# Performance work log

Measured on AMD Instinct MI355X. Metric: run time of the kernel, lower is better.

Reference implementation:

```python
import jax, jax.numpy as jnp
import numpy as np

CHUNK = 128  # time_chunk_size from init_kwargs
EPS = 1e-8


def _forward(v, k, alpha, q):
    # v: (T,B,d), k/alpha/q: (T,B,n)
    T, B, d = v.shape
    n = k.shape[-1]
    nc = T // CHUNK  # T assumed divisible by CHUNK
    vr = v.reshape(nc, CHUNK, B, d)
    kr = k.reshape(nc, CHUNK, B, n)
    ar = alpha.reshape(nc, CHUNK, B, n)
    qr = q.reshape(nc, CHUNK, B, n)

    def step(S_prev, xs):
        vc, kc, ac, qc = xs  # (C,B,d), (C,B,n), ...
        outer = jnp.einsum('tbd,tbn->tbdn', vc, kc)          # (C,B,d,n)
        log_a = jnp.log(jnp.clip(ac, EPS))
        log_cp = jnp.cumsum(log_a, axis=0)                   # (C,B,n)
        cp = jnp.exp(log_cp)
        decay = cp / (cp[-1:] + EPS)                         # normalized per chunk
        S_local = jnp.cumsum(outer * decay[:, :, None, :], axis=0)
        prefix = jnp.exp(log_cp[0])                          # (B,n) decay of first step
        S_local = S_local + (S_prev * prefix[:, None, :])[None]
        y = jnp.einsum('tbdn,tbn->tbd', S_local, qc)         # (C,B,d)
        return S_local[-1], y

    S0 = jnp.zeros((B, d, n), v.dtype)
    _, ys = jax.lax.scan(step, S0, (vr, kr, ar, qr))
    return ys.reshape(T, B, d)


def setup_inputs() -> dict:
    key = jax.random.key(0)
    k1, k2, k3, k4 = jax.random.split(key, 4)
    T, B, d, n = 2048, 4, 256, 256
    return {
        'v': jax.random.normal(k1, (T, B, d), jnp.float32),
        'k': jax.random.normal(k2, (T, B, n), jnp.float32),
        'alpha': jax.random.uniform(k3, (T, B, n), jnp.float32),
        'q': jax.random.normal(k4, (T, B, n), jnp.float32),
    }


def reference(v, k, alpha, q):
    return _forward(v, k, alpha, q)
```

## Files before the change

### kernel.cpp

```cpp
#include <hip/hip_runtime.h>
#include <math.h>

typedef unsigned short u16;
typedef unsigned int u32;
typedef __bf16 bf16x8 __attribute__((ext_vector_type(8)));
typedef float f32x4 __attribute__((ext_vector_type(4)));

#define BB   4
#define DD   256
#define NN   256
#define CH   128
#define NCH  16
#define EPSF 1e-8f

#define WS_QB  0u
#define WS_VT  (4u<<20)
#define WS_WT  (8u<<20)
#define WS_WN  (12u<<20)
#define WS_AST (16u<<20)
#define WS_SPT (18u<<20)
#define WS_PF  (26u<<20)
#define WS_UT  (28u<<20)

__device__ __forceinline__ u16 f2bf(float x) {
  u32 u = __float_as_uint(x);
  u32 r = (u + 0x7fffu + ((u >> 16) & 1u)) >> 16;
  return (u16)r;
}
__device__ __forceinline__ float bf2f(u32 lo16) {
  return __uint_as_float(lo16 << 16);
}

__device__ __forceinline__ void gload16(void* lds, const void* g) {
  __builtin_amdgcn_global_load_lds((const __attribute__((address_space(1))) void*)g,
                                   (__attribute__((address_space(3))) void*)lds, 16, 0, 0);
}

__device__ __forceinline__ void stage_tile(u16* lds, const u16* g, int rowstride) {
  int tid = threadIdx.x;
#pragma unroll
  for (int h = 0; h < 2; h++) {
    int ci = tid + h * 256;
    int r = ci >> 3, sl = ci & 7;
    const u16* src = g + (size_t)r * rowstride + ((sl ^ (r & 7)) << 3);
    gload16(lds + (size_t)ci * 8, src);
  }
}

__device__ __forceinline__ void read_frags(const u16* buf, int rbase, int lane,
                                           bf16x8 (&f)[2][2]) {
#pragma unroll
  for (int i = 0; i < 2; i++)
#pragma unroll
    for (int ks = 0; ks < 2; ks++) {
      int r = rbase + i * 16 + (lane & 15);
      int slot = ((ks << 2) + (lane >> 4)) ^ (r & 7);
      f[i][ks] = *reinterpret_cast<const bf16x8*>(buf + r * 64 + slot * 8);
    }
}

__device__ __forceinline__ void mma_step(const u16* Ab, const u16* Bb, int rm, int cn,
                                         int lane, f32x4 (&acc)[2][2]) {
  bf16x8 a[2][2], b[2][2];
  read_frags(Ab, rm, lane, a);
  read_frags(Bb, cn, lane, b);
#pragma unroll
  for (int mf = 0; mf < 2; mf++)
#pragma unroll
    for (int nf = 0; nf < 2; nf++)
#pragma unroll
      for (int ks = 0; ks < 2; ks++)
        acc[mf][nf] = __builtin_amdgcn_mfma_f32_16x16x32_bf16(a[mf][ks], b[nf][ks],
                                                              acc[mf][nf], 0, 0, 0);
}

__global__ __launch_bounds__(256) void k_prep(const float* __restrict__ q,
                                              const float* __restrict__ v,
                                              const float* __restrict__ kin,
                                              const float* __restrict__ alpha,
                                              u16* __restrict__ qb,
                                              u16* __restrict__ vT,
                                              u16* __restrict__ wT,
                                              u16* __restrict__ wn,
                                              float* __restrict__ pf) {
  __shared__ __align__(16) char smem[64 * 136 * 2];
  int bid = blockIdx.x;
  int tid = threadIdx.x;
  if (bid < 1024) {
    int ng = bid & 15, b = (bid >> 4) & 3, c = bid >> 6;
    int nn = tid & 15, seg = tid >> 4;
    int n = ng * 16 + nn;
    int cb = c * BB + b;
    const int stride = BB * NN;
    size_t gbase = ((size_t)(c * CH + seg * 8) * stride) + b * NN + n;
    float lg[8], kv[8];
    float a0 = 0.f, run = 0.f;
#pragma unroll
    for (int i = 0; i < 8; i++) {
      float av = fmaxf(alpha[gbase + (size_t)i * stride], EPSF);
      kv[i] = kin[gbase + (size_t)i * stride];
      if (i == 0) a0 = av;
      run += __logf(av);
      lg[i] = run;
    }
    float (*tot)[17] = (float(*)[17])smem;
    tot[seg][nn] = run;
    __syncthreads();
    float prefix = 0.f, total = 0.f;
#pragma unroll
    for (int j = 0; j < 16; j++) {
      float tv = tot[j][nn];
      if (j < seg) prefix += tv;
      total += tv;
    }
    float rden = 1.f / (__expf(total) + EPSF);
    union { u16 u[8]; uint4 v4; } pk;
    u16* wnrow = wn + (size_t)cb * (CH * NN) + n;
#pragma unroll
    for (int i = 0; i < 8; i++) {
      float cp = __expf(prefix + lg[i]);
      u16 h = f2bf(kv[i] * (cp * rden));
      pk.u[i] = h;
      wnrow[(size_t)(seg * 8 + i) * NN] = h;
    }
    *(uint4*)(wT + (size_t)cb * (NN * CH) + (size_t)n * CH + seg * 8) = pk.v4;
    if (seg == 0) pf[cb * NN + n] = a0;
  } else if (bid < 1280) {
    int b2 = bid - 1024;
    int dt = b2 & 3, cb = b2 >> 2;
    int c = cb >> 2, b = cb & 3;
    int d0 = dt * 64;
    u16* vt = (u16*)smem;
    int sr = tid >> 4, chd = tid & 15;
#pragma unroll
    for (int p = 0; p < 8; p++) {
      int s = p * 16 + sr;
      float4 x = *(const float4*)&v[((size_t)(c * CH + s) * BB + b) * DD + d0 + chd * 4];
      int dbase = chd * 4;
      vt[(dbase + 0) * 136 + s] = f2bf(x.x);
      vt[(dbase + 1) * 136 + s] = f2bf(x.y);
      vt[(dbase + 2) * 136 + s] = f2bf(x.z);
      vt[(dbase + 3) * 136 + s] = f2bf(x.w);
    }
    __syncthreads();
    int dr = tid >> 2, ch = tid & 3;
    const uint4* srcl = (const uint4*)&vt[dr * 136 + ch * 32];
    uint4 a0 = srcl[0], a1 = srcl[1], a2 = srcl[2], a3 = srcl[3];
    uint4* dst = (uint4*)&vT[((size_t)cb * DD + d0 + dr) * CH + ch * 32];
    dst[0] = a0; dst[1] = a1; dst[2] = a2; dst[3] = a3;
  } else {
    size_t gid = (size_t)(bid - 1280) * 256 + tid;
    const float4* src = (const float4*)q + gid * 2;
    float4 x = src[0], z = src[1];
    union { u16 u[8]; uint4 v4; } pk;
    pk.u[0] = f2bf(x.x); pk.u[1] = f2bf(x.y); pk.u[2] = f2bf(x.z); pk.u[3] = f2bf(x.w);
    pk.u[4] = f2bf(z.x); pk.u[5] = f2bf(z.y); pk.u[6] = f2bf(z.z); pk.u[7] = f2bf(z.w);
    ((uint4*)qb)[gid] = pk.v4;
  }
}

__global__ __launch_bounds__(256) void k_utas(const u16* __restrict__ vT,
                                              const u16* __restrict__ wT,
                                              const u16* __restrict__ qb,
                                              const u16* __restrict__ wn,
                                              u16* __restrict__ utb,
                                              u16* __restrict__ asT) {
  __shared__ u16 Al[2][4096], Bl[2][4096];
  int bid = blockIdx.x;
  int tid = threadIdx.x, lane = tid & 63, wv = tid >> 6;
  int rm = (wv >> 1) * 32, cn = (wv & 1) * 32;
  if (bid < 1024) {
    int nt = bid & 3, dt = (bid >> 2) & 3, cb = bid >> 4;
    const u16* A = vT + ((size_t)cb * DD + dt * 64) * CH;
    const u16* B = wT + ((size_t)cb * NN + nt * 64) * CH;
    f32x4 acc[2][2] = {};
    stage_tile(Al[0], A, CH); stage_tile(Al[1], A + 64, CH);
    stage_tile(Bl[0], B, CH); stage_tile(Bl[1], B + 64, CH);
    __syncthreads();
    mma_step(Al[0], Bl[0], rm, cn, lane, acc);
    mma_step(Al[1], Bl[1], rm, cn, lane, acc);
    u16* out = utb + ((size_t)cb * DD + dt * 64) * NN + nt * 64;
#pragma unroll
    for (int mf = 0; mf < 2; mf++)
#pragma unroll
      for (int nf = 0; nf < 2; nf++)
#pragma unroll
        for (int r = 0; r < 4; r++) {
          int row = rm + mf * 16 + (lane >> 4) * 4 + r;
          int col = cn + nf * 16 + (lane & 15);
          out[(size_t)row * NN + col] = f2bf(acc[mf][nf][r]);
        }
  } else {
    int bid2 = bid - 1024;
    int tile = bid2 % 3;
    int cb = bid2 / 3;
    int ti = (tile == 0) ? 0 : 1;
    int si = (tile == 2) ? 1 : 0;
    int t0 = ti * 64, s0 = si * 64;
    int c = cb >> 2, b = cb & 3;
    const u16* A = qb + ((size_t)(c * CH + t0) * BB + b) * NN;
    const u16* B = wn + (size_t)cb * (CH * NN) + (size_t)s0 * NN;
    f32x4 acc[2][2] = {};
    stage_tile(Al[0], A, BB * NN); stage_tile(Bl[0], B, NN);
    __syncthreads();
    for (int st = 0; st < 4; st++) {
      int nx = st + 1;
      if (nx < 4) {
        stage_tile(Al[nx & 1], A + nx * 64, BB * NN);
        stage_tile(Bl[nx & 1], B + nx * 64, NN);
      }
      mma_step(Al[st & 1], Bl[st & 1], rm, cn, lane, acc);
      __syncthreads();
    }
    u16* outb = asT + (size_t)cb * (CH * CH);
#pragma unroll
    for (int mf = 0; mf < 2; mf++)
#pragma unroll
      for (int nf = 0; nf < 2; nf++)
#pragma unroll
        for (int r = 0; r < 4; r++) {
          int t = t0 + rm + mf * 16 + (lane >> 4) * 4 + r;
          int s = s0 + cn + nf * 16 + (lane & 15);
          float val = (s <= t) ? acc[mf][nf][r] : 0.f;
          outb[(size_t)t * CH + s] = f2bf(val);
        }
  }
}

__global__ __launch_bounds__(256) void k_scan(const u32* __restrict__ utT2,
                                              const float* __restrict__ pf,
                                              u32* __restrict__ sptT2) {
  int id = blockIdx.x * 256 + threadIdx.x;
  int nh = id & 127, dd = (id >> 7) & 255, b = id >> 15;
  u32 u[NCH];
  float2 pp[NCH];
#pragma unroll
  for (int ch = 0; ch < NCH; ch++) {
    int cb = ch * BB + b;
    u[ch] = utT2[((size_t)cb * DD + dd) * 128 + nh];
    pp[ch] = *(const float2*)&pf[cb * NN + nh * 2];
  }
  float S0 = 0.f, S1 = 0.f;
#pragma unroll
  for (int ch = 0; ch < NCH; ch++) {
    int cb = ch * BB + b;
    float Sp0 = S0 * pp[ch].x, Sp1 = S1 * pp[ch].y;
    sptT2[((size_t)cb * DD + dd) * 128 + nh] = (u32)f2bf(Sp0) | ((u32)f2bf(Sp1) << 16);
    S0 = Sp0 + bf2f(u[ch] & 0xffffu);
    S1 = Sp1 + bf2f(u[ch] >> 16);
  }
}

__global__ __launch_bounds__(256) void k_out(const u16* __restrict__ qb,
                                             const u16* __restrict__ sptT,
                                             const u16* __restrict__ asT,
                                             const u16* __restrict__ vT,
                                             float* __restrict__ y) {
  int bid = blockIdx.x;
  int dt = bid & 3, tt = (bid >> 2) & 1, cb = bid >> 3;
  int c = cb >> 2, b = cb & 3;
  int t0 = tt * 64, d0 = dt * 64;
  int tid = threadIdx.x, lane = tid & 63, wv = tid >> 6;
  int rm = (wv >> 1) * 32, cn = (wv & 1) * 32;
  const u16* A1 = qb + ((size_t)(c * CH + t0) * BB + b) * NN;
  const u16* B1 = sptT + ((size_t)cb * DD + d0) * NN;
  const u16* A2 = asT + (size_t)cb * (CH * CH) + (size_t)t0 * CH;
  const u16* B2 = vT + ((size_t)cb * DD + d0) * CH;
  __shared__ u16 Al[2][4096], Bl[2][4096];
  f32x4 acc[2][2] = {};
  int nst = 5 + tt;
  stage_tile(Al[0], A1, BB * NN); stage_tile(Bl[0], B1, NN);
  __syncthreads();
  for (int st = 0; st < nst; st++) {
    int nx = st + 1;
    if (nx < 4) {
      stage_tile(Al[nx & 1], A1 + nx * 64, BB * NN);
      stage_tile(Bl[nx & 1], B1 + nx * 64, NN);
    } else if (nx < nst) {
      stage_tile(Al[nx & 1], A2 + (nx - 4) * 64, CH);
      stage_tile(Bl[nx & 1], B2 + (nx - 4) * 64, CH);
    }
    mma_step(Al[st & 1], Bl[st & 1], rm, cn, lane, acc);
    __syncthreads();
  }
  float* out = y + ((size_t)(c * CH + t0) * BB + b) * DD + d0;
#pragma unroll
  for (int mf = 0; mf < 2; mf++)
#pragma unroll
    for (int nf = 0; nf < 2; nf++)
#pragma unroll
      for (int r = 0; r < 4; r++) {
        int row = rm + mf * 16 + (lane >> 4) * 4 + r;
        int col = cn + nf * 16 + (lane & 15);
        out[(size_t)row * (BB * DD) + col] = acc[mf][nf][r];
      }
}

extern "C" void kernel_launch(void* const* d_in, const int* in_sizes, int n_in,
                              void* d_out, int out_size, void* d_ws, size_t ws_size,
                              hipStream_t stream) {
  const float* v = (const float*)d_in[0];
  const float* k = (const float*)d_in[1];
  const float* alpha = (const float*)d_in[2];
  const float* q = (const float*)d_in[3];
  float* y = (float*)d_out;
  char* ws = (char*)d_ws;
  u16* qb = (u16*)(ws + WS_QB);
  u16* vT = (u16*)(ws + WS_VT);
  u16* wT = (u16*)(ws + WS_WT);
  u16* wn = (u16*)(ws + WS_WN);
  u16* asT = (u16*)(ws + WS_AST);
  u16* sptT = (u16*)(ws + WS_SPT);
  float* pf = (float*)(ws + WS_PF);
  u16* utb = (u16*)(ws + WS_UT);

  k_prep<<<2304, 256, 0, stream>>>(q, v, k, alpha, qb, vT, wT, wn, pf);
  k_utas<<<1216, 256, 0, stream>>>(vT, wT, qb, wn, utb, asT);
  k_scan<<<512, 256, 0, stream>>>((const u32*)utb, pf, (u32*)sptT);
  k_out<<<512, 256, 0, stream>>>(qb, sptT, asT, vT, y);
}
```

Before: 40.47 us.

## Move intra-chunk attention GEMM into scan kernel and swizzle blocks across XCDs

Splits the combined chunk-state/attention kernel so that the small masked q·w attention GEMM now runs in the same launch as the inter-chunk scan. This lets the latency-bound scan and the attention tiles share the GPU instead of the attention tiles lengthening the state GEMM launch. It also remaps block indices so that neighbouring blocks land on the same XCD in the state GEMM and output kernels, which is meant to improve L2 locality. The main risk is load imbalance between the two heterogeneous block types sharing the scan launch.

```diff
diff --git a/kernel.cpp b/kernel.cpp
--- a/kernel.cpp
+++ b/kernel.cpp
@@ -29,6 +29,10 @@
 }
 __device__ __forceinline__ float bf2f(u32 lo16) {
   return __uint_as_float(lo16 << 16);
+}
+
+__device__ __forceinline__ int xcd_swz(int bid, int nwg) {
+  return (bid & 7) * (nwg >> 3) + (bid >> 3);
 }
 
 __device__ __forceinline__ void gload16(void* lds, const void* g) {
@@ -159,41 +163,49 @@
   }
 }
 
-__global__ __launch_bounds__(256) void k_utas(const u16* __restrict__ vT,
-                                              const u16* __restrict__ wT,
-                                              const u16* __restrict__ qb,
-                                              const u16* __restrict__ wn,
-                                              u16* __restrict__ utb,
-                                              u16* __restrict__ asT) {
+__global__ __launch_bounds__(256) void k_ut(const u16* __restrict__ vT,
+                                            const u16* __restrict__ wT,
+                                            u16* __restrict__ utb) {
+  __shared__ u16 Al[2][4096], Bl[2][4096];
+  int bid = xcd_swz(blockIdx.x, 1024);
+  int tid = threadIdx.x, lane = tid & 63, wv = tid >> 6;
+  int rm = (wv >> 1) * 32, cn = (wv & 1) * 32;
+  int nt = bid & 3, dt = (bid >> 2) & 3, cb = bid >> 4;
+  const u16* A = vT + ((size_t)cb * DD + dt * 64) * CH;
+  const u16* B = wT + ((size_t)cb * NN + nt * 64) * CH;
+  f32x4 acc[2][2] = {};
+  stage_tile(Al[0], A, CH); stage_tile(Al[1], A + 64, CH);
+  stage_tile(Bl[0], B, CH); stage_tile(Bl[1], B + 64, CH);
+  __syncthreads();
+  mma_step(Al[0], Bl[0], rm, cn, lane, acc);
+  mma_step(Al[1], Bl[1], rm, cn, lane, acc);
+  u16* out = utb + ((size_t)cb * DD + dt * 64) * NN + nt * 64;
+#pragma unroll
+  for (int mf = 0; mf < 2; mf++)
+#pragma unroll
+    for (int nf = 0; nf < 2; nf++)
+#pragma unroll
+      for (int r = 0; r < 4; r++) {
+        int row = rm + mf * 16 + (lane >> 4) * 4 + r;
+        int col = cn + nf * 16 + (lane & 15);
+        out[(size_t)row * NN + col] = f2bf(acc[mf][nf][r]);
+      }
+}
+
+__global__ __launch_bounds__(256) void k_scanas(const u16* __restrict__ qb,
+                                                const u16* __restrict__ wn,
+                                                const u32* __restrict__ utT2,
+                                                const float* __restrict__ pf,
+                                                u16* __restrict__ asT,
+                                                u32* __restrict__ sptT2) {
   __shared__ u16 Al[2][4096], Bl[2][4096];
   int bid = blockIdx.x;
-  int tid = threadIdx.x, lane = tid & 63, wv = tid >> 6;
-  int rm = (wv >> 1) * 32, cn = (wv & 1) * 32;
-  if (bid < 1024) {
-    int nt = bid & 3, dt = (bid >> 2) & 3, cb = bid >> 4;
-    const u16* A = vT + ((size_t)cb * DD + dt * 64) * CH;
-    const u16* B = wT + ((size_t)cb * NN + nt * 64) * CH;
-    f32x4 acc[2][2] = {};
-    stage_tile(Al[0], A, CH); stage_tile(Al[1], A + 64, CH);
-    stage_tile(Bl[0], B, CH); stage_tile(Bl[1], B + 64, CH);
-    __syncthreads();
-    mma_step(Al[0], Bl[0], rm, cn, lane, acc);
-    mma_step(Al[1], Bl[1], rm, cn, lane, acc);
-    u16* out = utb + ((size_t)cb * DD + dt * 64) * NN + nt * 64;
-#pragma unroll
-    for (int mf = 0; mf < 2; mf++)
-#pragma unroll
-      for (int nf = 0; nf < 2; nf++)
-#pragma unroll
-        for (int r = 0; r < 4; r++) {
-          int row = rm + mf * 16 + (lane >> 4) * 4 + r;
-          int col = cn + nf * 16 + (lane & 15);
-          out[(size_t)row * NN + col] = f2bf(acc[mf][nf][r]);
-        }
-  } else {
-    int bid2 = bid - 1024;
-    int tile = bid2 % 3;
-    int cb = bid2 / 3;
+  int tid = threadIdx.x;
+  if (bid < 192) {
+    int lane = tid & 63, wv = tid >> 6;
+    int rm = (wv >> 1) * 32, cn = (wv & 1) * 32;
+    int tile = bid % 3;
+    int cb = bid / 3;
     int ti = (tile == 0) ? 0 : 1;
     int si = (tile == 2) ? 1 : 0;
     int t0 = ti * 64, s0 = si * 64;
@@ -224,30 +236,26 @@
           float val = (s <= t) ? acc[mf][nf][r] : 0.f;
           outb[(size_t)t * CH + s] = f2bf(val);
         }
-  }
-}
-
-__global__ __launch_bounds__(256) void k_scan(const u32* __restrict__ utT2,
-                                              const float* __restrict__ pf,
-                                              u32* __restrict__ sptT2) {
-  int id = blockIdx.x * 256 + threadIdx.x;
-  int nh = id & 127, dd = (id >> 7) & 255, b = id >> 15;
-  u32 u[NCH];
-  float2 pp[NCH];
-#pragma unroll
-  for (int ch = 0; ch < NCH; ch++) {
-    int cb = ch * BB + b;
-    u[ch] = utT2[((size_t)cb * DD + dd) * 128 + nh];
-    pp[ch] = *(const float2*)&pf[cb * NN + nh * 2];
-  }
-  float S0 = 0.f, S1 = 0.f;
-#pragma unroll
-  for (int ch = 0; ch < NCH; ch++) {
-    int cb = ch * BB + b;
-    float Sp0 = S0 * pp[ch].x, Sp1 = S1 * pp[ch].y;
-    sptT2[((size_t)cb * DD + dd) * 128 + nh] = (u32)f2bf(Sp0) | ((u32)f2bf(Sp1) << 16);
-    S0 = Sp0 + bf2f(u[ch] & 0xffffu);
-    S1 = Sp1 + bf2f(u[ch] >> 16);
+  } else {
+    int id = (bid - 192) * 256 + tid;
+    int nh = id & 127, dd = (id >> 7) & 255, b = id >> 15;
+    u32 u[NCH];
+    float2 pp[NCH];
+#pragma unroll
+    for (int ch = 0; ch < NCH; ch++) {
+      int cb = ch * BB + b;
+      u[ch] = utT2[((size_t)cb * DD + dd) * 128 + nh];
+      pp[ch] = *(const float2*)&pf[cb * NN + nh * 2];
+    }
+    float S0 = 0.f, S1 = 0.f;
+#pragma unroll
+    for (int ch = 0; ch < NCH; ch++) {
+      int cb = ch * BB + b;
+      float Sp0 = S0 * pp[ch].x, Sp1 = S1 * pp[ch].y;
+      sptT2[((size_t)cb * DD + dd) * 128 + nh] = (u32)f2bf(Sp0) | ((u32)f2bf(Sp1) << 16);
+      S0 = Sp0 + bf2f(u[ch] & 0xffffu);
+      S1 = Sp1 + bf2f(u[ch] >> 16);
+    }
   }
 }
 
@@ -256,7 +264,7 @@
                                              const u16* __restrict__ asT,
                                              const u16* __restrict__ vT,
                                              float* __restrict__ y) {
-  int bid = blockIdx.x;
+  int bid = xcd_swz(blockIdx.x, 512);
   int dt = bid & 3, tt = (bid >> 2) & 1, cb = bid >> 3;
   int c = cb >> 2, b = cb & 3;
   int t0 = tt * 64, d0 = dt * 64;
@@ -315,7 +323,7 @@
   u16* utb = (u16*)(ws + WS_UT);
 
   k_prep<<<2304, 256, 0, stream>>>(q, v, k, alpha, qb, vT, wT, wn, pf);
-  k_utas<<<1216, 256, 0, stream>>>(vT, wT, qb, wn, utb, asT);
-  k_scan<<<512, 256, 0, stream>>>((const u32*)utb, pf, (u32*)sptT);
+  k_ut<<<1024, 256, 0, stream>>>(vT, wT, utb);
+  k_scanas<<<704, 256, 0, stream>>>(qb, wn, (const u32*)utb, pf, asT, (u32*)sptT);
   k_out<<<512, 256, 0, stream>>>(qb, sptT, asT, vT, y);
 }
```

New measurement: 35.79 us. -11.6%, faster.
